# Kernel optimization log

Hardware: AMD Instinct MI355X
Metric: run time of the kernel (lower is better)

## Reference

```python
import jax, jax.numpy as jnp
import numpy as np

N = 200000   # total atoms in batched graph
E = 3200000  # total bonds (directed edges)
B = 512      # number of graphs / sequences
L = 1000     # miRNA sequence length


def _gcn(x, W, b, src, dst, dis):
    # PyG GCNConv: add self-loops, symmetric normalization D^-1/2 A D^-1/2
    h = x @ W                                   # [N, Fout]
    msg = (dis[src] * dis[dst])[:, None] * h[src]
    agg = jax.ops.segment_sum(msg, dst, num_segments=x.shape[0])
    return agg + (dis * dis)[:, None] * h + b   # self-loop term + bias


def _conv1d(x, k, b):
    # x: [B, C, L], k: [O, I, K]  (torch Conv1d, VALID padding)
    y = jax.lax.conv_general_dilated(x, k, (1,), 'VALID',
                                     dimension_numbers=('NCH', 'OIH', 'NCH'))
    return y + b[None, :, None]


def _mp3(x):
    # torch MaxPool1d(3): window 3, stride 3, floor
    return jax.lax.reduce_window(x, -jnp.inf, jax.lax.max, (1, 1, 3), (1, 1, 3), 'VALID')


def setup_inputs() -> dict:
    key = jax.random.key(0)
    ks = jax.random.split(key, 24)
    w = lambda k, s: (jax.random.normal(k, s, jnp.float32) * 0.1)
    p = {}
    p['x'] = jax.random.normal(ks[0], (N, 4), jnp.float32)
    p['edge_index'] = jax.random.randint(ks[1], (2, E), 0, N, jnp.int32)
    p['batch'] = (jnp.arange(N, dtype=jnp.int32) * B // N).astype(jnp.int32)  # every graph non-empty
    p['target'] = jax.random.normal(ks[2], (B, L, 5), jnp.float32)
    # GCN layers 4->4->8->16
    p['W1'] = w(ks[3], (4, 4));    p['b1'] = jnp.zeros(4, jnp.float32)
    p['W2'] = w(ks[4], (4, 8));    p['b2'] = jnp.zeros(8, jnp.float32)
    p['W3'] = w(ks[5], (8, 16));   p['b3'] = jnp.zeros(16, jnp.float32)
    p['Wg1'] = w(ks[6], (16, 1024)); p['bg1'] = jnp.zeros(1024, jnp.float32)
    p['Wg2'] = w(ks[7], (1024, 128)); p['bg2'] = jnp.zeros(128, jnp.float32)
    # CNN stack on sequences, kernels [O, I, 8]
    p['K1'] = w(ks[8], (32, 5, 8));   p['cb1'] = jnp.zeros(32, jnp.float32)
    p['K2'] = w(ks[9], (64, 32, 8));  p['cb2'] = jnp.zeros(64, jnp.float32)
    p['K3'] = w(ks[10], (128, 64, 8)); p['cb3'] = jnp.zeros(128, jnp.float32)
    p['Wxt'] = w(ks[11], (128, 128)); p['bxt'] = jnp.zeros(128, jnp.float32)
    # fusion head
    p['Wf1'] = w(ks[12], (256, 1024)); p['bf1'] = jnp.zeros(1024, jnp.float32)
    p['Wf2'] = w(ks[13], (1024, 512)); p['bf2'] = jnp.zeros(512, jnp.float32)
    p['Wo'] = w(ks[14], (512, 2));     p['bo'] = jnp.zeros(2, jnp.float32)
    return p


def reference(x, edge_index, batch, target, W1, b1, W2, b2, W3, b3,
              Wg1, bg1, Wg2, bg2, K1, cb1, K2, cb2, K3, cb3,
              Wxt, bxt, Wf1, bf1, Wf2, bf2, Wo, bo):
    src, dst = edge_index[0], edge_index[1]
    deg = jax.ops.segment_sum(jnp.ones(src.shape[0], x.dtype), dst,
                              num_segments=x.shape[0]) + 1.0  # +1 self-loop
    dis = jax.lax.rsqrt(deg)
    # Graph branch (dropout is identity in eval)
    h = jax.nn.relu(_gcn(x, W1, b1, src, dst, dis))
    h = jax.nn.relu(_gcn(h, W2, b2, src, dst, dis))
    h = jax.nn.relu(_gcn(h, W3, b3, src, dst, dis))
    g = jax.ops.segment_max(h, batch, num_segments=B)  # global_max_pool
    g = jax.nn.relu(g @ Wg1 + bg1)
    g = g @ Wg2 + bg2
    # Sequence branch
    t = jnp.transpose(target, (0, 2, 1))  # [B, 5, L]
    c = _mp3(jax.nn.relu(_conv1d(t, K1, cb1)))
    c = _mp3(jax.nn.relu(_conv1d(c, K2, cb2)))
    c = _mp3(jax.nn.relu(_conv1d(c, K3, cb3)))
    c = jnp.mean(c, axis=2)               # [B, 128]
    c = jax.nn.relu(c @ Wxt + bxt)
    # Fusion head
    xc = jnp.concatenate([g, c], axis=1)  # [B, 256]
    xc = jax.nn.relu(xc @ Wf1 + bf1)
    xc = jax.nn.relu(xc @ Wf2 + bf2)
    return xc @ Wo + bo                    # [B, 2]
```

## Files before the change

kernel.cpp:

```cpp
#include <hip/hip_runtime.h>
#include <hip/hip_fp16.h>
#include <cstddef>

#define NA 200000
#define NE 3200000
#define NB 512
#define NBKT 256
#define BKTN 782
#define BKTCAP 16384
#define NEPB 3200

typedef _Float16 hv2 __attribute__((ext_vector_type(2)));
typedef _Float16 half8 __attribute__((ext_vector_type(8)));
typedef float floatx4 __attribute__((ext_vector_type(4)));
union UH2 { unsigned u; __half2 h; hv2 v; };
__device__ __forceinline__ float4 h4f(unsigned a, unsigned b) {
    UH2 x, y; x.u = a; y.u = b;
    float2 fa = __half22float2(x.h), fb = __half22float2(y.h);
    return make_float4(fa.x, fa.y, fb.x, fb.y);
}
__device__ __forceinline__ unsigned f2h(float a, float b) {
    UH2 r; r.h = __float22half2_rn(make_float2(a, b));
    return r.u;
}

__global__ void k_init(unsigned* g, int* gcursor,
                       float* gvec, const float* __restrict__ bg2,
                       float* xf2, const float* __restrict__ bf2,
                       float* xf1, const float* __restrict__ bf1,
                       const float* __restrict__ K2, const float* __restrict__ K3,
                       __half* __restrict__ Wt2, __half* __restrict__ Wt3) {
    int i = blockIdx.x * blockDim.x + threadIdx.x;
    if (i < NB * 16) g[i] = 0u;
    if (i < NBKT) gcursor[i] = i * BKTCAP;
    if (i < NB * 128) gvec[i] = bg2[i & 127];
    if (i < NB * 512) xf2[i] = bf2[i & 511];
    if (i < NB * 1024) xf1[i] = bf1[i & 1023];
    if (i < 64 * 32 * 8) {
        int o = i >> 8, rem = i & 255, c = rem >> 3, kk = rem & 7;
        Wt2[(o << 8) + (kk << 5) + c] = __float2half(K2[i]);
    }
    if (i < 128 * 64 * 8) {
        int o = i >> 9, rem = i & 511, c = rem >> 3, kk = rem & 7;
        Wt3[(o << 9) + (kk << 6) + c] = __float2half(K3[i]);
    }
}

template<int CIN, int COUT, int OBLK, int LIN, int PITCH, int POUT, int NTT>
__device__ __forceinline__ void dev_conv1(int b, int oy,
        const float* __restrict__ in, const float* __restrict__ Kw,
        const float* __restrict__ bias, __half* __restrict__ out,
        float* s_in) {
    constexpr int SPO = 256 / OBLK;
    constexpr int PT = (NTT < 4) ? NTT : 4;
    constexpr int NPASS = (NTT + PT - 1) / PT;
    for (int idx = threadIdx.x; idx < CIN * PITCH; idx += 256) s_in[idx] = 0.f;
    __syncthreads();
    for (int idx = threadIdx.x; idx < LIN * CIN; idx += 256) {
        int p = idx / CIN, c = idx - p * CIN;
        s_in[c * PITCH + p] = in[(size_t)b * (LIN * CIN) + idx];
    }
    __syncthreads();
    int ol = threadIdx.x / SPO;
    int s  = threadIdx.x - ol * SPO;
    int o  = oy * OBLK + ol;
    float bo = bias[o];
    const float* wrow = Kw + (size_t)o * CIN * 8;
    for (int pass = 0; pass < NPASS; pass++) {
        float acc[PT][12];
#pragma unroll
        for (int tt = 0; tt < PT; tt++)
#pragma unroll
            for (int j = 0; j < 12; j++) acc[tt][j] = 0.f;
        bool vld[PT]; int tgs[PT];
#pragma unroll
        for (int tt = 0; tt < PT; tt++) {
            int ta = pass * PT + tt;
            int tg = s + SPO * ta;
            tgs[tt] = tg;
            vld[tt] = (ta < NTT) && (4 * tg < POUT);
        }
        for (int i = 0; i < CIN; i++) {
            float wa[8];
            const float4* wp = (const float4*)(wrow + (size_t)i * 8);
            *(float4*)&wa[0] = wp[0];
            *(float4*)&wa[4] = wp[1];
#pragma unroll
            for (int tt = 0; tt < PT; tt++) {
                if (vld[tt]) {
                    const float4* xr = (const float4*)&s_in[i * PITCH + 12 * tgs[tt]];
                    float xa[20];
#pragma unroll
                    for (int q = 0; q < 5; q++) *(float4*)&xa[4 * q] = xr[q];
#pragma unroll
                    for (int j = 0; j < 12; j++) {
                        float sm = acc[tt][j];
#pragma unroll
                        for (int k = 0; k < 8; k++) sm = fmaf(xa[j + k], wa[k], sm);
                        acc[tt][j] = sm;
                    }
                }
            }
        }
#pragma unroll
        for (int tt = 0; tt < PT; tt++) {
            if (vld[tt]) {
#pragma unroll
                for (int p = 0; p < 4; p++) {
                    int P = 4 * tgs[tt] + p;
                    if (P < POUT) {
                        float m = fmaxf(fmaxf(acc[tt][3 * p], acc[tt][3 * p + 1]), acc[tt][3 * p + 2]);
                        out[((size_t)b * COUT + o) * POUT + P] = __float2half(fmaxf(m + bo, 0.f));
                    }
                }
            }
        }
    }
}

__device__ __forceinline__ void dev_conv2_mfma(int b,
        const __half* __restrict__ pool1, const __half* __restrict__ Wt2,
        const float* __restrict__ cb2, __half* __restrict__ pool2t,
        char* smem) {
    __half* sT   = (__half*)smem;
    __half* outS = (__half*)smem;
    const __half* inp = pool1 + (size_t)b * (32 * 331);
    for (int idx = threadIdx.x; idx < 32 * 331; idx += 256) {
        int c = idx / 331;
        int p = idx - c * 331;
        sT[p * 40 + c] = inp[idx];
    }
    __syncthreads();
    int lane = threadIdx.x & 63, wv = threadIdx.x >> 6;
    int l15 = lane & 15, lg = lane >> 4;
    int mtBeg = wv * 5;
    int nmt = (wv == 3) ? 6 : 5;
    const floatx4 FZ = {0.f, 0.f, 0.f, 0.f};
    floatx4 acc[6][4];
#pragma unroll
    for (int mi = 0; mi < 6; mi++)
#pragma unroll
        for (int nt = 0; nt < 4; nt++) acc[mi][nt] = FZ;
    const half8* WB = (const half8*)Wt2;
    for (int s = 0; s < 8; s++) {
        half8 bfr[4];
#pragma unroll
        for (int nt = 0; nt < 4; nt++)
            bfr[nt] = WB[(nt * 16 + l15) * 32 + s * 4 + lg];
        half8 afr[6];
#pragma unroll
        for (int mi = 0; mi < 6; mi++) {
            if (mi < nmt) {
                int row = (mtBeg + mi) * 16 + l15 + s;
                afr[mi] = *(const half8*)(sT + row * 40 + lg * 8);
            }
        }
#pragma unroll
        for (int mi = 0; mi < 6; mi++) {
            if (mi < nmt) {
#pragma unroll
                for (int nt = 0; nt < 4; nt++)
                    acc[mi][nt] = __builtin_amdgcn_mfma_f32_16x16x32_f16(
                        afr[mi], bfr[nt], acc[mi][nt], 0, 0, 0);
            }
        }
    }
    __syncthreads();
    float bo[4];
#pragma unroll
    for (int nt = 0; nt < 4; nt++) bo[nt] = cb2[nt * 16 + l15];
#pragma unroll
    for (int mi = 0; mi < 6; mi++) {
        if (mi < nmt) {
#pragma unroll
            for (int nt = 0; nt < 4; nt++) {
                int o = nt * 16 + l15;
#pragma unroll
                for (int r = 0; r < 4; r++) {
                    int p = (mtBeg + mi) * 16 + lg * 4 + r;
                    float v = fmaxf(acc[mi][nt][r] + bo[nt], 0.f);
                    outS[p * 68 + o] = __float2half(v);
                }
            }
        }
    }
    __syncthreads();
    __half* op = pool2t + (size_t)b * (108 * 64);
    for (int idx = threadIdx.x; idx < 108 * 64; idx += 256) {
        int P = idx >> 6, o = idx & 63;
        float v0 = __half2float(outS[(3 * P) * 68 + o]);
        float v1 = __half2float(outS[(3 * P + 1) * 68 + o]);
        float v2 = __half2float(outS[(3 * P + 2) * 68 + o]);
        op[idx] = __float2half(fmaxf(fmaxf(v0, v1), v2));
    }
}

__device__ __forceinline__ void dev_conv3_mfma(int b, int nh,
        const __half* __restrict__ pool2t, const __half* __restrict__ Wt3,
        const float* __restrict__ cb3, float* __restrict__ pool3,
        char* smem) {
    __half* sT  = (__half*)smem;
    float* outS = (float*)smem;
    const uint4* inp = (const uint4*)(pool2t + (size_t)b * (108 * 64));
    for (int t = threadIdx.x; t < 108 * 8; t += 256) {
        int r = t >> 3, s8 = t & 7;
        *(uint4*)(sT + r * 72 + s8 * 8) = inp[t];
    }
    __syncthreads();
    int lane = threadIdx.x & 63, wv = threadIdx.x >> 6;
    int l15 = lane & 15, lg = lane >> 4;
    int mtBeg = wv * 2;
    int nmt = (wv == 3) ? 1 : 2;
    const floatx4 FZ = {0.f, 0.f, 0.f, 0.f};
    floatx4 acc[2][4];
#pragma unroll
    for (int mi = 0; mi < 2; mi++)
#pragma unroll
        for (int nt = 0; nt < 4; nt++) acc[mi][nt] = FZ;
    const half8* WB = (const half8*)Wt3;
    for (int s = 0; s < 16; s++) {
        half8 afr[2];
#pragma unroll
        for (int mi = 0; mi < 2; mi++) {
            if (mi < nmt) {
                int row = (mtBeg + mi) * 16 + l15 + (s >> 1);
                afr[mi] = *(const half8*)(sT + row * 72 + (s & 1) * 32 + lg * 8);
            }
        }
#pragma unroll
        for (int nt = 0; nt < 4; nt++) {
            half8 bfr = WB[((nh * 4 + nt) * 16 + l15) * 64 + s * 4 + lg];
            acc[0][nt] = __builtin_amdgcn_mfma_f32_16x16x32_f16(
                afr[0], bfr, acc[0][nt], 0, 0, 0);
            if (nmt > 1)
                acc[1][nt] = __builtin_amdgcn_mfma_f32_16x16x32_f16(
                    afr[1], bfr, acc[1][nt], 0, 0, 0);
        }
    }
    __syncthreads();
    float bo[4];
#pragma unroll
    for (int nt = 0; nt < 4; nt++) bo[nt] = cb3[(nh * 4 + nt) * 16 + l15];
    float* op = pool3 + (size_t)b * (33 * 128);
    for (int pp = 0; pp < 3; pp++) {
        int t0 = 3 * pp;
#pragma unroll
        for (int mi = 0; mi < 2; mi++) {
            int tile = mtBeg + mi;
            if (mi < nmt && tile >= t0 && tile < t0 + 3) {
#pragma unroll
                for (int nt = 0; nt < 4; nt++) {
                    int ol = nt * 16 + l15;
#pragma unroll
                    for (int r = 0; r < 4; r++) {
                        int p = tile * 16 + lg * 4 + r;
                        if (p < 100)
                            outS[(p - 48 * pp) * 68 + ol] =
                                fmaxf(acc[mi][nt][r] + bo[nt], 0.f);
                    }
                }
            }
        }
        __syncthreads();
        int nP = (pp == 2) ? 1 : 16;
        for (int idx = threadIdx.x; idx < nP * 64; idx += 256) {
            int Pl = idx >> 6, ol = idx & 63;
            int P = 16 * pp + Pl;
            int p = 3 * P - 48 * pp;
            float v0 = outS[p * 68 + ol];
            float v1 = outS[(p + 1) * 68 + ol];
            float v2 = outS[(p + 2) * 68 + ol];
            op[P * 128 + (nh << 6) + ol] = fmaxf(fmaxf(v0, v1), v2);
        }
        __syncthreads();
    }
}

__global__ __launch_bounds__(256) void k_A(
        const int* __restrict__ src, const int* __restrict__ dst,
        int* __restrict__ gcursor, unsigned* __restrict__ stage,
        const float* __restrict__ tgt, const float* __restrict__ K1,
        const float* __restrict__ cb1, __half* __restrict__ pool1) {
    __shared__ __align__(16) char smem[20160];
    int bx = blockIdx.x;
    if (bx >= 1000) {
        dev_conv1<5, 32, 16, 1000, 1008, 331, 6>(bx - 1000, 0, tgt, K1, cb1,
                                                 pool1, (float*)smem);
        return;
    }
    int* hcnt  = (int*)smem;
    int* hbase = hcnt + 256;
    int* lbase = hbase + 256;
    unsigned* sbuf = (unsigned*)(lbase + 256);
    unsigned char* sbkt = (unsigned char*)(sbuf + NEPB);
    int t = threadIdx.x;
    int e0 = bx * NEPB;
    hcnt[t] = 0;
    __syncthreads();
    const int4* d4 = (const int4*)(dst + e0);
    for (int i = t; i < NEPB / 4; i += 256) {
        int4 d = d4[i];
        atomicAdd(&hcnt[d.x / BKTN], 1);
        atomicAdd(&hcnt[d.y / BKTN], 1);
        atomicAdd(&hcnt[d.z / BKTN], 1);
        atomicAdd(&hcnt[d.w / BKTN], 1);
    }
    __syncthreads();
    int myc = hcnt[t];
    hbase[t] = atomicAdd(&gcursor[t], myc);
    __syncthreads();
#pragma unroll
    for (int off = 1; off < 256; off <<= 1) {
        int u = (t >= off) ? hcnt[t - off] : 0;
        __syncthreads();
        hcnt[t] += u;
        __syncthreads();
    }
    lbase[t] = hcnt[t] - myc;
    hcnt[t] = 0;
    __syncthreads();
    const int4* s4 = (const int4*)(src + e0);
    for (int i = t; i < NEPB / 4; i += 256) {
        int4 d = d4[i];
        int4 s = s4[i];
        int ds[4] = {d.x, d.y, d.z, d.w};
        int ss[4] = {s.x, s.y, s.z, s.w};
#pragma unroll
        for (int j = 0; j < 4; j++) {
            int bkt = ds[j] / BKTN;
            int dloc = ds[j] - bkt * BKTN;
            int k = atomicAdd(&hcnt[bkt], 1);
            int pos = lbase[bkt] + k;
            sbuf[pos] = ((unsigned)dloc << 18) | (unsigned)ss[j];
            sbkt[pos] = (unsigned char)bkt;
        }
    }
    __syncthreads();
    for (int i = t; i < NEPB; i += 256) {
        unsigned v = sbuf[i];
        int bkt = sbkt[i];
        stage[hbase[bkt] + (i - lbase[bkt])] = v;
    }
}

__global__ __launch_bounds__(256) void k_Bp(
        const unsigned* __restrict__ stage, const int* __restrict__ gcursor,
        int* __restrict__ rowptr, int* __restrict__ cnt, int* __restrict__ csr,
        const float* __restrict__ x, float4* __restrict__ dt1,
        const float* __restrict__ tgt, const float* __restrict__ K1,
        const float* __restrict__ cb1, __half* __restrict__ pool1) {
    __shared__ __align__(16) char smem[20160];
    __shared__ int sbase;
    int bx = blockIdx.x;
    if (bx >= NBKT) {
        dev_conv1<5, 32, 16, 1000, 1008, 331, 6>(bx - NBKT, 1, tgt, K1, cb1,
                                                 pool1, (float*)smem);
        return;
    }
    int* lcnt    = (int*)smem;
    int* lpos    = lcnt + BKTN;
    int* partial = lpos + BKTN;
    int t = threadIdx.x;
    int bkt = bx;
    int tot = gcursor[t] - t * BKTCAP;
    partial[t] = tot;
    __syncthreads();
#pragma unroll
    for (int off = 1; off < 256; off <<= 1) {
        int u = (t >= off) ? partial[t - off] : 0;
        __syncthreads();
        partial[t] += u;
        __syncthreads();
    }
    if (t == 0) sbase = (bkt == 0) ? 0 : partial[bkt - 1];
    __syncthreads();
    int base = sbase;
    int n0 = bkt * BKTN;
    int ncnt = (NA - n0 < BKTN) ? (NA - n0) : BKTN;
    int eBeg = bkt * BKTCAP;
    int eCnt = gcursor[bkt] - eBeg;
    for (int i = t; i < BKTN; i += 256) lcnt[i] = 0;
    __syncthreads();
    for (int i = t; i < eCnt; i += 256)
        atomicAdd(&lcnt[stage[eBeg + i] >> 18], 1);
    __syncthreads();
    int mysum = 0;
#pragma unroll
    for (int j = 0; j < 4; j++) {
        int node = 4 * t + j;
        if (node < ncnt) mysum += lcnt[node];
    }
    partial[t] = mysum;
    __syncthreads();
#pragma unroll
    for (int off = 1; off < 256; off <<= 1) {
        int u = (t >= off) ? partial[t - off] : 0;
        __syncthreads();
        partial[t] += u;
        __syncthreads();
    }
    int running = partial[t] - mysum;
#pragma unroll
    for (int j = 0; j < 4; j++) {
        int node = 4 * t + j;
        if (node < ncnt) {
            lpos[node] = running;
            rowptr[n0 + node] = base + running;
            cnt[n0 + node] = lcnt[node];
            running += lcnt[node];
        }
    }
    __syncthreads();
    for (int i = t; i < eCnt; i += 256) {
        unsigned v = stage[eBeg + i];
        int dloc = v >> 18;
        int s = v & 0x3FFFF;
        int k = atomicAdd(&lpos[dloc], 1);
        csr[base + k] = s;
    }
    for (int i = t; i < ncnt; i += 256) {
        int n = n0 + i;
        float4 p = ((const float4*)x)[n];
        float dv = rsqrtf((float)lcnt[i] + 1.0f);
        dt1[n] = make_float4(dv * p.x, dv * p.y, dv * p.z, dv * p.w);
    }
}

__global__ __launch_bounds__(256) void k_B(
        const __half* __restrict__ pool1, const __half* __restrict__ Wt2,
        const float* __restrict__ cb2, __half* __restrict__ pool2t,
        const float4* __restrict__ dt1, const int* __restrict__ rowptr,
        const int* __restrict__ cnt, const int* __restrict__ csr,
        const float* __restrict__ W1, const float* __restrict__ b1,
        float4* __restrict__ dt2) {
    __shared__ __align__(16) char smem[45696];
    int bx = blockIdx.x;
    if (bx < 512) {
        dev_conv2_mfma(bx, pool1, Wt2, cb2, pool2t, smem);
        return;
    }
    __shared__ float sW[16];
    if (threadIdx.x < 16) sW[threadIdx.x] = W1[threadIdx.x];
    __syncthreads();
    int n = (bx - 512) * 256 + threadIdx.x;
    if (n >= NA) return;
    int cn = cnt[n];
    float dv = rsqrtf((float)cn + 1.0f);
    const int* row = csr + rowptr[n];
    float4 acc = dt1[n];
    int e = 0;
    for (; e + 7 < cn; e += 8) {
        int idx[8];
#pragma unroll
        for (int u = 0; u < 8; u++) idx[u] = row[e + u];
        float4 v[8];
#pragma unroll
        for (int u = 0; u < 8; u++) v[u] = dt1[idx[u]];
#pragma unroll
        for (int u = 0; u < 8; u++) {
            acc.x += v[u].x; acc.y += v[u].y; acc.z += v[u].z; acc.w += v[u].w;
        }
    }
    for (; e < cn; e++) {
        float4 v = dt1[row[e]];
        acc.x += v.x; acc.y += v.y; acc.z += v.z; acc.w += v.w;
    }
    const float4 bq = *(const float4*)b1;
    float a[4] = {acc.x, acc.y, acc.z, acc.w};
    float bb[4] = {bq.x, bq.y, bq.z, bq.w};
    float o[4];
#pragma unroll
    for (int f = 0; f < 4; f++) {
        float s = 0.f;
#pragma unroll
        for (int k = 0; k < 4; k++) s = fmaf(a[k], sW[k * 4 + f], s);
        o[f] = dv * fmaxf(fmaf(dv, s, bb[f]), 0.f);
    }
    dt2[n] = make_float4(o[0], o[1], o[2], o[3]);
}

__global__ __launch_bounds__(256, 8) void k_C(
        const __half* __restrict__ pool2t, const __half* __restrict__ Wt3,
        const float* __restrict__ cb3, float* __restrict__ pool3,
        const float4* __restrict__ dt2, const int* __restrict__ rowptr,
        const int* __restrict__ cnt, const int* __restrict__ csr,
        const float* __restrict__ W2, const float* __restrict__ b2,
        uint4* __restrict__ dt3) {
    __shared__ __align__(16) char smem[17280];
    int bx = blockIdx.x;
    if (bx < 1024) {
        dev_conv3_mfma(bx & 511, bx >> 9, pool2t, Wt3, cb3, pool3, smem);
        return;
    }
    __shared__ float sW[32];
    if (threadIdx.x < 32) sW[threadIdx.x] = W2[threadIdx.x];
    __syncthreads();
    int n = (bx - 1024) * 256 + threadIdx.x;
    if (n >= NA) return;
    int cn = cnt[n];
    float dv = rsqrtf((float)cn + 1.0f);
    const int* row = csr + rowptr[n];
    float4 acc = dt2[n];
    int e = 0;
    for (; e + 7 < cn; e += 8) {
        int idx[8];
#pragma unroll
        for (int u = 0; u < 8; u++) idx[u] = row[e + u];
        float4 v[8];
#pragma unroll
        for (int u = 0; u < 8; u++) v[u] = dt2[idx[u]];
#pragma unroll
        for (int u = 0; u < 8; u++) {
            acc.x += v[u].x; acc.y += v[u].y; acc.z += v[u].z; acc.w += v[u].w;
        }
    }
    for (; e < cn; e++) {
        float4 v = dt2[row[e]];
        acc.x += v.x; acc.y += v.y; acc.z += v.z; acc.w += v.w;
    }
    float a[4] = {acc.x, acc.y, acc.z, acc.w};
    float o[8];
#pragma unroll
    for (int f = 0; f < 8; f++) {
        float s = 0.f;
#pragma unroll
        for (int k = 0; k < 4; k++) s = fmaf(a[k], sW[k * 8 + f], s);
        o[f] = dv * fmaxf(fmaf(dv, s, b2[f]), 0.f);
    }
    dt3[n] = make_uint4(f2h(o[0], o[1]), f2h(o[2], o[3]),
                        f2h(o[4], o[5]), f2h(o[6], o[7]));
}

__global__ __launch_bounds__(256) void k_D(
        const uint4* __restrict__ dt3, const int* __restrict__ rowptr,
        const int* __restrict__ cnt, const int* __restrict__ csr,
        const float* __restrict__ W3, const float* __restrict__ b3,
        const int* __restrict__ batch, unsigned* __restrict__ g,
        const float* __restrict__ pool3, const float* __restrict__ Wxt,
        const float* __restrict__ bxt, float* __restrict__ cx) {
    int bx = blockIdx.x;
    if (bx >= 782) {
        __shared__ float sa[8 * 128];
        int b0 = (bx - 782) * 8;
        for (int t = threadIdx.x; t < 8 * 128; t += 256) {
            int gg = t >> 7, k = t & 127;
            const float* r = pool3 + (size_t)(b0 + gg) * (33 * 128) + k;
            float s = 0.f;
#pragma unroll
            for (int p = 0; p < 33; p++) s += r[p * 128];
            sa[t] = s * (1.f / 33.f);
        }
        __syncthreads();
        int j = threadIdx.x;
        if (j >= 128) return;
        float bj = bxt[j];
        float acc[8];
#pragma unroll
        for (int gg = 0; gg < 8; gg++) acc[gg] = bj;
#pragma unroll 4
        for (int k = 0; k < 128; k++) {
            float w = Wxt[(size_t)k * 128 + j];
#pragma unroll
            for (int gg = 0; gg < 8; gg++) acc[gg] = fmaf(sa[gg * 128 + k], w, acc[gg]);
        }
#pragma unroll
        for (int gg = 0; gg < 8; gg++)
            cx[(size_t)(b0 + gg) * 128 + j] = fmaxf(acc[gg], 0.f);
        return;
    }
    __shared__ float sW[128];
    __shared__ unsigned sg[32];
    __shared__ int sbmin;
    int id = bx;
    if (threadIdx.x < 128) sW[threadIdx.x] = W3[threadIdx.x];
    if (threadIdx.x < 32) sg[threadIdx.x] = 0u;
    if (threadIdx.x == 0) sbmin = batch[id * 256];
    __syncthreads();
    int n = id * 256 + threadIdx.x;
    if (n < NA) {
        int cn = cnt[n];
        float dv = rsqrtf((float)cn + 1.0f);
        const int* row = csr + rowptr[n];
        uint4 sv = dt3[n];
        float4 lo = h4f(sv.x, sv.y), hi = h4f(sv.z, sv.w);
        float a0 = lo.x, a1 = lo.y, a2 = lo.z, a3 = lo.w;
        float a4 = hi.x, a5 = hi.y, a6 = hi.z, a7 = hi.w;
        int e = 0;
        for (; e + 3 < cn; e += 4) {
            uint4 p0 = dt3[row[e]],     p1 = dt3[row[e + 1]];
            uint4 p2 = dt3[row[e + 2]], p3 = dt3[row[e + 3]];
            float4 l0 = h4f(p0.x, p0.y), h0 = h4f(p0.z, p0.w);
            float4 l1 = h4f(p1.x, p1.y), h1 = h4f(p1.z, p1.w);
            float4 l2 = h4f(p2.x, p2.y), h2 = h4f(p2.z, p2.w);
            float4 l3 = h4f(p3.x, p3.y), h3v = h4f(p3.z, p3.w);
            a0 += (l0.x + l1.x) + (l2.x + l3.x);
            a1 += (l0.y + l1.y) + (l2.y + l3.y);
            a2 += (l0.z + l1.z) + (l2.z + l3.z);
            a3 += (l0.w + l1.w) + (l2.w + l3.w);
            a4 += (h0.x + h1.x) + (h2.x + h3v.x);
            a5 += (h0.y + h1.y) + (h2.y + h3v.y);
            a6 += (h0.z + h1.z) + (h2.z + h3v.z);
            a7 += (h0.w + h1.w) + (h2.w + h3v.w);
        }
        for (; e < cn; e++) {
            uint4 p = dt3[row[e]];
            float4 l = h4f(p.x, p.y), h = h4f(p.z, p.w);
            a0 += l.x; a1 += l.y; a2 += l.z; a3 += l.w;
            a4 += h.x; a5 += h.y; a6 += h.z; a7 += h.w;
        }
        float af[8] = {a0, a1, a2, a3, a4, a5, a6, a7};
        int rb = batch[n] - sbmin;
        if (rb > 1) rb = 1;
#pragma unroll
        for (int f = 0; f < 16; f++) {
            float s = 0.f;
#pragma unroll
            for (int k = 0; k < 8; k++) s = fmaf(af[k], sW[k * 16 + f], s);
            float r = fmaxf(fmaf(dv, s, b3[f]), 0.f);
            atomicMax(&sg[rb * 16 + f], __float_as_uint(r));
        }
    }
    __syncthreads();
    if (threadIdx.x < 32) {
        unsigned v = sg[threadIdx.x];
        int rb2 = threadIdx.x >> 4, f = threadIdx.x & 15;
        int bbn = sbmin + rb2;
        if (v != 0u && bbn < NB) atomicMax(&g[bbn * 16 + f], v);
    }
}

__global__ __launch_bounds__(256) void k_head_g(
        const float* __restrict__ g, const float* __restrict__ Wg1,
        const float* __restrict__ bg1, float* __restrict__ gp1) {
    __shared__ float sa[8 * 16];
    int bx = blockIdx.x;
    int b0 = (bx >> 2) * 8;
    if (threadIdx.x < 128)
        sa[threadIdx.x] = g[b0 * 16 + threadIdx.x];
    __syncthreads();
    int j = (bx & 3) * 256 + threadIdx.x;
    float bj = bg1[j];
    float acc[8];
#pragma unroll
    for (int gg = 0; gg < 8; gg++) acc[gg] = bj;
#pragma unroll
    for (int k = 0; k < 16; k++) {
        float w = Wg1[(size_t)k * 1024 + j];
#pragma unroll
        for (int gg = 0; gg < 8; gg++) acc[gg] = fmaf(sa[gg * 16 + k], w, acc[gg]);
    }
#pragma unroll
    for (int gg = 0; gg < 8; gg++)
        gp1[(size_t)(b0 + gg) * 1024 + j] = fmaxf(acc[gg], 0.f);
}

__global__ __launch_bounds__(256) void k_gvec_ks(
        const float* __restrict__ gp1, const float* __restrict__ Wg2,
        float* __restrict__ gvec) {
    __shared__ float sa[8 * 128];
    int k0 = blockIdx.x * 128;
    int b0 = blockIdx.y * 8;
    for (int t = threadIdx.x; t < 8 * 128; t += 256) {
        int gg = t >> 7, k = t & 127;
        sa[t] = gp1[(size_t)(b0 + gg) * 1024 + k0 + k];
    }
    __syncthreads();
    int j  = threadIdx.x & 127;
    int kh = (threadIdx.x >> 7) * 64;
    const float* Wp = Wg2 + (size_t)(k0 + kh) * 128 + j;
    float acc[8];
#pragma unroll
    for (int gg = 0; gg < 8; gg++) acc[gg] = 0.f;
    for (int k = 0; k < 64; k += 16) {
        float w[16];
#pragma unroll
        for (int u = 0; u < 16; u++) w[u] = Wp[(size_t)(k + u) * 128];
#pragma unroll
        for (int u = 0; u < 16; u++) {
#pragma unroll
            for (int gg = 0; gg < 8; gg++)
                acc[gg] = fmaf(sa[gg * 128 + kh + k + u], w[u], acc[gg]);
        }
    }
#pragma unroll
    for (int gg = 0; gg < 8; gg++)
        atomicAdd(&gvec[(size_t)(b0 + gg) * 128 + j], acc[gg]);
}

__global__ __launch_bounds__(256) void k_cat2(
        const float* __restrict__ gvec, const float* __restrict__ cx,
        const float* __restrict__ Wf1, float* __restrict__ xf1) {
    __shared__ float sa[8 * 128];
    int jx = blockIdx.x & 3;
    int kh = blockIdx.x >> 2;
    int b0 = blockIdx.y * 8;
    const float* A = kh ? cx : gvec;
    for (int t = threadIdx.x; t < 8 * 128; t += 256) {
        int gg = t >> 7, k = t & 127;
        sa[t] = A[(size_t)(b0 + gg) * 128 + k];
    }
    __syncthreads();
    int j = jx * 256 + threadIdx.x;
    const float* Wp = Wf1 + (size_t)(kh * 128) * 1024 + j;
    float acc[8];
#pragma unroll
    for (int gg = 0; gg < 8; gg++) acc[gg] = 0.f;
    for (int k = 0; k < 128; k += 16) {
        float w[16];
#pragma unroll
        for (int u = 0; u < 16; u++) w[u] = Wp[(size_t)(k + u) * 1024];
#pragma unroll
        for (int u = 0; u < 16; u++) {
#pragma unroll
            for (int gg = 0; gg < 8; gg++)
                acc[gg] = fmaf(sa[gg * 128 + k + u], w[u], acc[gg]);
        }
    }
#pragma unroll
    for (int gg = 0; gg < 8; gg++)
        atomicAdd(&xf1[(size_t)(b0 + gg) * 1024 + j], acc[gg]);
}

__global__ __launch_bounds__(256) void k_xf2_ks(
        const float* __restrict__ xf1, const float* __restrict__ Wf2,
        float* __restrict__ xf2) {
    __shared__ float sa[8 * 256];
    int jb = blockIdx.x & 1;
    int k0 = (blockIdx.x >> 1) * 256;
    int b0 = blockIdx.y * 8;
    for (int t = threadIdx.x; t < 8 * 256; t += 256) {
        int gg = t >> 8, k = t & 255;
        sa[t] = fmaxf(xf1[(size_t)(b0 + gg) * 1024 + k0 + k], 0.f);
    }
    __syncthreads();
    int j = jb * 256 + threadIdx.x;
    const float* Wp = Wf2 + (size_t)k0 * 512 + j;
    float acc[8];
#pragma unroll
    for (int gg = 0; gg < 8; gg++) acc[gg] = 0.f;
    for (int k = 0; k < 256; k += 16) {
        float w[16];
#pragma unroll
        for (int u = 0; u < 16; u++) w[u] = Wp[(size_t)(k + u) * 512];
#pragma unroll
        for (int u = 0; u < 16; u++) {
#pragma unroll
            for (int gg = 0; gg < 8; gg++)
                acc[gg] = fmaf(sa[gg * 256 + k + u], w[u], acc[gg]);
        }
    }
#pragma unroll
    for (int gg = 0; gg < 8; gg++)
        atomicAdd(&xf2[(size_t)(b0 + gg) * 512 + j], acc[gg]);
}

__global__ __launch_bounds__(256) void k_dense_out(
        const float* __restrict__ A, const float* __restrict__ W,
        const float* __restrict__ bias, float* __restrict__ out) {
    int idx = blockIdx.x * 256 + threadIdx.x;
    if (idx >= NB * 2) return;
    int b = idx >> 1, j = idx & 1;
    float s = bias[j];
    const float4* A4 = (const float4*)(A + (size_t)b * 512);
    for (int k4 = 0; k4 < 128; k4 += 8) {
        float4 av[8];
#pragma unroll
        for (int u = 0; u < 8; u++) av[u] = A4[k4 + u];
#pragma unroll
        for (int u = 0; u < 8; u++) {
            int kb = (k4 + u) * 4;
            s = fmaf(fmaxf(av[u].x, 0.f), W[(kb + 0) * 2 + j], s);
            s = fmaf(fmaxf(av[u].y, 0.f), W[(kb + 1) * 2 + j], s);
            s = fmaf(fmaxf(av[u].z, 0.f), W[(kb + 2) * 2 + j], s);
            s = fmaf(fmaxf(av[u].w, 0.f), W[(kb + 3) * 2 + j], s);
        }
    }
    out[idx] = s;
}

extern "C" void kernel_launch(void* const* d_in, const int* in_sizes, int n_in,
                              void* d_out, int out_size, void* d_ws, size_t ws_size,
                              hipStream_t stream) {
    (void)in_sizes; (void)n_in; (void)out_size; (void)ws_size;
    const float* x   = (const float*)d_in[0];
    const int*  ei   = (const int*)d_in[1];
    const int*  batch= (const int*)d_in[2];
    const float* tgt = (const float*)d_in[3];
    const float* W1  = (const float*)d_in[4];  const float* b1  = (const float*)d_in[5];
    const float* W2  = (const float*)d_in[6];  const float* b2  = (const float*)d_in[7];
    const float* W3  = (const float*)d_in[8];  const float* b3  = (const float*)d_in[9];
    const float* Wg1 = (const float*)d_in[10]; const float* bg1 = (const float*)d_in[11];
    const float* Wg2 = (const float*)d_in[12]; const float* bg2 = (const float*)d_in[13];
    const float* K1  = (const float*)d_in[14]; const float* cb1 = (const float*)d_in[15];
    const float* K2  = (const float*)d_in[16]; const float* cb2 = (const float*)d_in[17];
    const float* K3  = (const float*)d_in[18]; const float* cb3 = (const float*)d_in[19];
    const float* Wxt = (const float*)d_in[20]; const float* bxt = (const float*)d_in[21];
    const float* Wf1 = (const float*)d_in[22]; const float* bf1 = (const float*)d_in[23];
    const float* Wf2 = (const float*)d_in[24]; const float* bf2 = (const float*)d_in[25];
    const float* Wo  = (const float*)d_in[26]; const float* bo  = (const float*)d_in[27];
    const int* srcp = ei;
    const int* dstp = ei + NE;

    float* ws = (float*)d_ws;
    float4* dt1 = (float4*)ws; ws += (size_t)NA * 4;
    float4* dt2 = (float4*)ws; ws += (size_t)NA * 4;
    uint4*  dt3 = (uint4*)ws;  ws += (size_t)NA * 4;
    float* g     = ws; ws += NB * 16;
    float* gp1   = ws; ws += NB * 1024;
    float* gvec  = ws; ws += NB * 128;
    float* cx    = ws; ws += NB * 128;
    float* xf1   = ws; ws += NB * 1024;
    float* xf2   = ws; ws += NB * 512;
    __half* pool1 = (__half*)ws; ws += (size_t)NB * 32 * 331;
    __half* pool2t = (__half*)ws; ws += (size_t)NB * 64 * 108;
    float* pool3 = ws; ws += (size_t)NB * 128 * 33;
    __half* Wt2 = (__half*)ws; ws += 64 * 256 / 2;
    __half* Wt3 = (__half*)ws; ws += 128 * 512 / 2;
    int*   cnt    = (int*)ws; ws += NA;
    int*   rowptr = (int*)ws; ws += NA;
    int*   csr    = (int*)ws; ws += NE;
    int*   gcursor= (int*)ws; ws += NBKT;
    unsigned* stage = (unsigned*)ws; ws += (size_t)NBKT * BKTCAP;

    dim3 blk(256);

    k_init<<<2048, blk, 0, stream>>>((unsigned*)g, gcursor, gvec, bg2, xf2, bf2,
                                     xf1, bf1, K2, K3, Wt2, Wt3);
    k_A<<<1512, blk, 0, stream>>>(srcp, dstp, gcursor, stage, tgt, K1, cb1, pool1);
    k_Bp<<<768, blk, 0, stream>>>(stage, gcursor, rowptr, cnt, csr, x, dt1,
                                  tgt, K1, cb1, pool1);
    k_B<<<1294, blk, 0, stream>>>(pool1, Wt2, cb2, pool2t,
                                  dt1, rowptr, cnt, csr, W1, b1, dt2);
    k_C<<<1806, blk, 0, stream>>>(pool2t, Wt3, cb3, pool3,
                                  dt2, rowptr, cnt, csr, W2, b2, dt3);
    k_D<<<846, blk, 0, stream>>>(dt3, rowptr, cnt, csr, W3, b3,
                                 batch, (unsigned*)g, pool3, Wxt, bxt, cx);

    k_head_g<<<256, blk, 0, stream>>>(g, Wg1, bg1, gp1);
    k_gvec_ks<<<dim3(8, 64), blk, 0, stream>>>(gp1, Wg2, gvec);
    k_cat2<<<dim3(8, 64), blk, 0, stream>>>(gvec, cx, Wf1, xf1);
    k_xf2_ks<<<dim3(8, 64), blk, 0, stream>>>(xf1, Wf2, xf2);
    k_dense_out<<<4, blk, 0, stream>>>(xf2, Wo, bo, (float*)d_out);
}
```

Measured before the change: 409.1 us.

## Split each node's neighbor gather across four lanes with shuffle reduction in GCN layers

The three GCN aggregation kernels now give each node four threads instead of one. Each lane gathers a strided quarter of the CSR neighbors, partial sums are combined with xor-shuffles, and each lane computes and writes a slice of the output features. This targets load imbalance and poor memory-level parallelism from one thread walking a whole neighbor list, which averages about 16 edges. The cost is four times more blocks, redundant self-loads and shuffle overhead, and less unrolling per thread.

```diff
diff --git a/kernel.cpp b/kernel.cpp
--- a/kernel.cpp
+++ b/kernel.cpp
@@ -9,6 +9,7 @@
 #define BKTN 782
 #define BKTCAP 16384
 #define NEPB 3200
+#define NGB 3125
 
 typedef _Float16 hv2 __attribute__((ext_vector_type(2)));
 typedef _Float16 half8 __attribute__((ext_vector_type(8)));
@@ -432,7 +433,7 @@
         const float4* __restrict__ dt1, const int* __restrict__ rowptr,
         const int* __restrict__ cnt, const int* __restrict__ csr,
         const float* __restrict__ W1, const float* __restrict__ b1,
-        float4* __restrict__ dt2) {
+        float* __restrict__ dt2f) {
     __shared__ __align__(16) char smem[45696];
     int bx = blockIdx.x;
     if (bx < 512) {
@@ -442,41 +443,35 @@
     __shared__ float sW[16];
     if (threadIdx.x < 16) sW[threadIdx.x] = W1[threadIdx.x];
     __syncthreads();
-    int n = (bx - 512) * 256 + threadIdx.x;
-    if (n >= NA) return;
+    int n   = (bx - 512) * 64 + (threadIdx.x >> 2);
+    int sub = threadIdx.x & 3;
     int cn = cnt[n];
     float dv = rsqrtf((float)cn + 1.0f);
     const int* row = csr + rowptr[n];
-    float4 acc = dt1[n];
-    int e = 0;
-    for (; e + 7 < cn; e += 8) {
-        int idx[8];
-#pragma unroll
-        for (int u = 0; u < 8; u++) idx[u] = row[e + u];
-        float4 v[8];
-#pragma unroll
-        for (int u = 0; u < 8; u++) v[u] = dt1[idx[u]];
-#pragma unroll
-        for (int u = 0; u < 8; u++) {
-            acc.x += v[u].x; acc.y += v[u].y; acc.z += v[u].z; acc.w += v[u].w;
-        }
-    }
-    for (; e < cn; e++) {
+    float4 selfv = dt1[n];
+    float4 acc = make_float4(0.f, 0.f, 0.f, 0.f);
+    if (sub == 0) acc = selfv;
+    int e = sub;
+    for (; e + 4 < cn; e += 8) {
+        float4 v0 = dt1[row[e]];
+        float4 v1 = dt1[row[e + 4]];
+        acc.x += v0.x + v1.x; acc.y += v0.y + v1.y;
+        acc.z += v0.z + v1.z; acc.w += v0.w + v1.w;
+    }
+    if (e < cn) {
         float4 v = dt1[row[e]];
         acc.x += v.x; acc.y += v.y; acc.z += v.z; acc.w += v.w;
     }
-    const float4 bq = *(const float4*)b1;
+    acc.x += __shfl_xor(acc.x, 1); acc.y += __shfl_xor(acc.y, 1);
+    acc.z += __shfl_xor(acc.z, 1); acc.w += __shfl_xor(acc.w, 1);
+    acc.x += __shfl_xor(acc.x, 2); acc.y += __shfl_xor(acc.y, 2);
+    acc.z += __shfl_xor(acc.z, 2); acc.w += __shfl_xor(acc.w, 2);
     float a[4] = {acc.x, acc.y, acc.z, acc.w};
-    float bb[4] = {bq.x, bq.y, bq.z, bq.w};
-    float o[4];
-#pragma unroll
-    for (int f = 0; f < 4; f++) {
-        float s = 0.f;
-#pragma unroll
-        for (int k = 0; k < 4; k++) s = fmaf(a[k], sW[k * 4 + f], s);
-        o[f] = dv * fmaxf(fmaf(dv, s, bb[f]), 0.f);
-    }
-    dt2[n] = make_float4(o[0], o[1], o[2], o[3]);
+    float s = 0.f;
+#pragma unroll
+    for (int k = 0; k < 4; k++) s = fmaf(a[k], sW[k * 4 + sub], s);
+    float o = dv * fmaxf(fmaf(dv, s, b1[sub]), 0.f);
+    dt2f[(size_t)n * 4 + sub] = o;
 }
 
 __global__ __launch_bounds__(256, 8) void k_C(
@@ -485,7 +480,7 @@
         const float4* __restrict__ dt2, const int* __restrict__ rowptr,
         const int* __restrict__ cnt, const int* __restrict__ csr,
         const float* __restrict__ W2, const float* __restrict__ b2,
-        uint4* __restrict__ dt3) {
+        unsigned* __restrict__ dt3u) {
     __shared__ __align__(16) char smem[17280];
     int bx = blockIdx.x;
     if (bx < 1024) {
@@ -495,40 +490,40 @@
     __shared__ float sW[32];
     if (threadIdx.x < 32) sW[threadIdx.x] = W2[threadIdx.x];
     __syncthreads();
-    int n = (bx - 1024) * 256 + threadIdx.x;
-    if (n >= NA) return;
+    int n   = (bx - 1024) * 64 + (threadIdx.x >> 2);
+    int sub = threadIdx.x & 3;
     int cn = cnt[n];
     float dv = rsqrtf((float)cn + 1.0f);
     const int* row = csr + rowptr[n];
-    float4 acc = dt2[n];
-    int e = 0;
-    for (; e + 7 < cn; e += 8) {
-        int idx[8];
-#pragma unroll
-        for (int u = 0; u < 8; u++) idx[u] = row[e + u];
-        float4 v[8];
-#pragma unroll
-        for (int u = 0; u < 8; u++) v[u] = dt2[idx[u]];
-#pragma unroll
-        for (int u = 0; u < 8; u++) {
-            acc.x += v[u].x; acc.y += v[u].y; acc.z += v[u].z; acc.w += v[u].w;
-        }
-    }
-    for (; e < cn; e++) {
+    float4 selfv = dt2[n];
+    float4 acc = make_float4(0.f, 0.f, 0.f, 0.f);
+    if (sub == 0) acc = selfv;
+    int e = sub;
+    for (; e + 4 < cn; e += 8) {
+        float4 v0 = dt2[row[e]];
+        float4 v1 = dt2[row[e + 4]];
+        acc.x += v0.x + v1.x; acc.y += v0.y + v1.y;
+        acc.z += v0.z + v1.z; acc.w += v0.w + v1.w;
+    }
+    if (e < cn) {
         float4 v = dt2[row[e]];
         acc.x += v.x; acc.y += v.y; acc.z += v.z; acc.w += v.w;
     }
+    acc.x += __shfl_xor(acc.x, 1); acc.y += __shfl_xor(acc.y, 1);
+    acc.z += __shfl_xor(acc.z, 1); acc.w += __shfl_xor(acc.w, 1);
+    acc.x += __shfl_xor(acc.x, 2); acc.y += __shfl_xor(acc.y, 2);
+    acc.z += __shfl_xor(acc.z, 2); acc.w += __shfl_xor(acc.w, 2);
     float a[4] = {acc.x, acc.y, acc.z, acc.w};
-    float o[8];
-#pragma unroll
-    for (int f = 0; f < 8; f++) {
-        float s = 0.f;
-#pragma unroll
-        for (int k = 0; k < 4; k++) s = fmaf(a[k], sW[k * 8 + f], s);
-        o[f] = dv * fmaxf(fmaf(dv, s, b2[f]), 0.f);
-    }
-    dt3[n] = make_uint4(f2h(o[0], o[1]), f2h(o[2], o[3]),
-                        f2h(o[4], o[5]), f2h(o[6], o[7]));
+    int f0 = 2 * sub;
+    float s0 = 0.f, s1 = 0.f;
+#pragma unroll
+    for (int k = 0; k < 4; k++) {
+        s0 = fmaf(a[k], sW[k * 8 + f0], s0);
+        s1 = fmaf(a[k], sW[k * 8 + f0 + 1], s1);
+    }
+    float o0 = dv * fmaxf(fmaf(dv, s0, b2[f0]), 0.f);
+    float o1 = dv * fmaxf(fmaf(dv, s1, b2[f0 + 1]), 0.f);
+    dt3u[(size_t)n * 4 + sub] = f2h(o0, o1);
 }
 
 __global__ __launch_bounds__(256) void k_D(
@@ -539,9 +534,9 @@
         const float* __restrict__ pool3, const float* __restrict__ Wxt,
         const float* __restrict__ bxt, float* __restrict__ cx) {
     int bx = blockIdx.x;
-    if (bx >= 782) {
+    if (bx >= NGB) {
         __shared__ float sa[8 * 128];
-        int b0 = (bx - 782) * 8;
+        int b0 = (bx - NGB) * 8;
         for (int t = threadIdx.x; t < 8 * 128; t += 256) {
             int gg = t >> 7, k = t & 127;
             const float* r = pool3 + (size_t)(b0 + gg) * (33 * 128) + k;
@@ -571,54 +566,58 @@
     __shared__ float sW[128];
     __shared__ unsigned sg[32];
     __shared__ int sbmin;
-    int id = bx;
     if (threadIdx.x < 128) sW[threadIdx.x] = W3[threadIdx.x];
     if (threadIdx.x < 32) sg[threadIdx.x] = 0u;
-    if (threadIdx.x == 0) sbmin = batch[id * 256];
-    __syncthreads();
-    int n = id * 256 + threadIdx.x;
-    if (n < NA) {
-        int cn = cnt[n];
-        float dv = rsqrtf((float)cn + 1.0f);
-        const int* row = csr + rowptr[n];
-        uint4 sv = dt3[n];
-        float4 lo = h4f(sv.x, sv.y), hi = h4f(sv.z, sv.w);
-        float a0 = lo.x, a1 = lo.y, a2 = lo.z, a3 = lo.w;
-        float a4 = hi.x, a5 = hi.y, a6 = hi.z, a7 = hi.w;
-        int e = 0;
-        for (; e + 3 < cn; e += 4) {
-            uint4 p0 = dt3[row[e]],     p1 = dt3[row[e + 1]];
-            uint4 p2 = dt3[row[e + 2]], p3 = dt3[row[e + 3]];
-            float4 l0 = h4f(p0.x, p0.y), h0 = h4f(p0.z, p0.w);
-            float4 l1 = h4f(p1.x, p1.y), h1 = h4f(p1.z, p1.w);
-            float4 l2 = h4f(p2.x, p2.y), h2 = h4f(p2.z, p2.w);
-            float4 l3 = h4f(p3.x, p3.y), h3v = h4f(p3.z, p3.w);
-            a0 += (l0.x + l1.x) + (l2.x + l3.x);
-            a1 += (l0.y + l1.y) + (l2.y + l3.y);
-            a2 += (l0.z + l1.z) + (l2.z + l3.z);
-            a3 += (l0.w + l1.w) + (l2.w + l3.w);
-            a4 += (h0.x + h1.x) + (h2.x + h3v.x);
-            a5 += (h0.y + h1.y) + (h2.y + h3v.y);
-            a6 += (h0.z + h1.z) + (h2.z + h3v.z);
-            a7 += (h0.w + h1.w) + (h2.w + h3v.w);
-        }
-        for (; e < cn; e++) {
-            uint4 p = dt3[row[e]];
-            float4 l = h4f(p.x, p.y), h = h4f(p.z, p.w);
-            a0 += l.x; a1 += l.y; a2 += l.z; a3 += l.w;
-            a4 += h.x; a5 += h.y; a6 += h.z; a7 += h.w;
-        }
-        float af[8] = {a0, a1, a2, a3, a4, a5, a6, a7};
-        int rb = batch[n] - sbmin;
-        if (rb > 1) rb = 1;
-#pragma unroll
-        for (int f = 0; f < 16; f++) {
-            float s = 0.f;
-#pragma unroll
-            for (int k = 0; k < 8; k++) s = fmaf(af[k], sW[k * 16 + f], s);
-            float r = fmaxf(fmaf(dv, s, b3[f]), 0.f);
-            atomicMax(&sg[rb * 16 + f], __float_as_uint(r));
-        }
+    if (threadIdx.x == 0) sbmin = batch[bx * 64];
+    __syncthreads();
+    int n   = bx * 64 + (threadIdx.x >> 2);
+    int sub = threadIdx.x & 3;
+    int cn = cnt[n];
+    float dv = rsqrtf((float)cn + 1.0f);
+    const int* row = csr + rowptr[n];
+    uint4 sv = dt3[n];
+    float4 slo = h4f(sv.x, sv.y), shi = h4f(sv.z, sv.w);
+    float a0 = 0.f, a1 = 0.f, a2 = 0.f, a3 = 0.f;
+    float a4 = 0.f, a5 = 0.f, a6 = 0.f, a7 = 0.f;
+    if (sub == 0) {
+        a0 = slo.x; a1 = slo.y; a2 = slo.z; a3 = slo.w;
+        a4 = shi.x; a5 = shi.y; a6 = shi.z; a7 = shi.w;
+    }
+    int e = sub;
+    for (; e + 4 < cn; e += 8) {
+        uint4 p0 = dt3[row[e]], p1 = dt3[row[e + 4]];
+        float4 l0 = h4f(p0.x, p0.y), h0 = h4f(p0.z, p0.w);
+        float4 l1 = h4f(p1.x, p1.y), h1 = h4f(p1.z, p1.w);
+        a0 += l0.x + l1.x; a1 += l0.y + l1.y;
+        a2 += l0.z + l1.z; a3 += l0.w + l1.w;
+        a4 += h0.x + h1.x; a5 += h0.y + h1.y;
+        a6 += h0.z + h1.z; a7 += h0.w + h1.w;
+    }
+    if (e < cn) {
+        uint4 p = dt3[row[e]];
+        float4 l = h4f(p.x, p.y), h = h4f(p.z, p.w);
+        a0 += l.x; a1 += l.y; a2 += l.z; a3 += l.w;
+        a4 += h.x; a5 += h.y; a6 += h.z; a7 += h.w;
+    }
+    a0 += __shfl_xor(a0, 1); a1 += __shfl_xor(a1, 1);
+    a2 += __shfl_xor(a2, 1); a3 += __shfl_xor(a3, 1);
+    a4 += __shfl_xor(a4, 1); a5 += __shfl_xor(a5, 1);
+    a6 += __shfl_xor(a6, 1); a7 += __shfl_xor(a7, 1);
+    a0 += __shfl_xor(a0, 2); a1 += __shfl_xor(a1, 2);
+    a2 += __shfl_xor(a2, 2); a3 += __shfl_xor(a3, 2);
+    a4 += __shfl_xor(a4, 2); a5 += __shfl_xor(a5, 2);
+    a6 += __shfl_xor(a6, 2); a7 += __shfl_xor(a7, 2);
+    float af[8] = {a0, a1, a2, a3, a4, a5, a6, a7};
+    int rb = batch[n] - sbmin;
+    if (rb > 1) rb = 1;
+#pragma unroll
+    for (int j = 0; j < 4; j++) {
+        int f = sub * 4 + j;
+        float s = 0.f;
+#pragma unroll
+        for (int k = 0; k < 8; k++) s = fmaf(af[k], sW[k * 16 + f], s);
+        float r = fmaxf(fmaf(dv, s, b3[f]), 0.f);
+        atomicMax(&sg[rb * 16 + f], __float_as_uint(r));
     }
     __syncthreads();
     if (threadIdx.x < 32) {
@@ -829,12 +828,12 @@
     k_A<<<1512, blk, 0, stream>>>(srcp, dstp, gcursor, stage, tgt, K1, cb1, pool1);
     k_Bp<<<768, blk, 0, stream>>>(stage, gcursor, rowptr, cnt, csr, x, dt1,
                                   tgt, K1, cb1, pool1);
-    k_B<<<1294, blk, 0, stream>>>(pool1, Wt2, cb2, pool2t,
-                                  dt1, rowptr, cnt, csr, W1, b1, dt2);
-    k_C<<<1806, blk, 0, stream>>>(pool2t, Wt3, cb3, pool3,
-                                  dt2, rowptr, cnt, csr, W2, b2, dt3);
-    k_D<<<846, blk, 0, stream>>>(dt3, rowptr, cnt, csr, W3, b3,
-                                 batch, (unsigned*)g, pool3, Wxt, bxt, cx);
+    k_B<<<512 + NGB, blk, 0, stream>>>(pool1, Wt2, cb2, pool2t,
+                                       dt1, rowptr, cnt, csr, W1, b1, (float*)dt2);
+    k_C<<<1024 + NGB, blk, 0, stream>>>(pool2t, Wt3, cb3, pool3,
+                                        dt2, rowptr, cnt, csr, W2, b2, (unsigned*)dt3);
+    k_D<<<NGB + 64, blk, 0, stream>>>(dt3, rowptr, cnt, csr, W3, b3,
+                                      batch, (unsigned*)g, pool3, Wxt, bxt, cx);
 
     k_head_g<<<256, blk, 0, stream>>>(g, Wg1, bg1, gp1);
     k_gvec_ks<<<dim3(8, 64), blk, 0, stream>>>(gp1, Wg2, gvec);
```

Measured after the change: 396.8 us. -3.0%, faster.
